# Kernel tuning notes

Measured on AMD Instinct MI355X. Metric: run time of the kernel, lower is better.

The kernel has to match this reference:

```python
import jax, jax.numpy as jnp
import numpy as np

VOCAB = 16000
DIM = 1024
B, T = 4, 2048


def setup_inputs() -> dict:
    key = jax.random.key(0)
    k_ids, k_emb, k_w, k_lw, k_lb = jax.random.split(key, 5)
    input_ids = jax.random.randint(k_ids, (B, T), 0, VOCAB)
    embed = jax.random.normal(k_emb, (VOCAB, DIM), dtype=jnp.float32)
    # w_state = I + 0.05 * (default Linear init ~ U(-1/sqrt(dim), 1/sqrt(dim)))
    bound = 1.0 / np.sqrt(DIM)
    w_state = jnp.eye(DIM, dtype=jnp.float32) + 0.05 * jax.random.uniform(
        k_w, (DIM, DIM), minval=-bound, maxval=bound, dtype=jnp.float32)
    lm_w = jax.random.uniform(k_lw, (VOCAB, DIM), minval=-bound, maxval=bound, dtype=jnp.float32)
    lm_b = jax.random.uniform(k_lb, (VOCAB,), minval=-bound, maxval=bound, dtype=jnp.float32)
    return {"input_ids": input_ids, "embed": embed, "w_state": w_state,
            "lm_w": lm_w, "lm_b": lm_b}


def reference(input_ids, embed, w_state, lm_w, lm_b):
    # h: [B, T, D]
    h = embed[input_ids]
    state0 = jnp.zeros((h.shape[0], h.shape[2]), dtype=h.dtype)

    def step(state, h_t):
        # nn.Linear: state @ W^T ; then add input injection
        new_state = state @ w_state.T + h_t
        return new_state, new_state

    # scan over time: inputs [T, B, D]
    _, outs = jax.lax.scan(step, state0, jnp.swapaxes(h, 0, 1))
    hidden = jnp.swapaxes(outs, 0, 1)  # [B, T, D]
    logits = hidden @ lm_w.T + lm_b    # [B, T, V]
    return logits
```

## Files before the change

kernel.cpp:

```cpp
#include <hip/hip_runtime.h>
#include <hip/hip_bf16.h>
#include <stdint.h>

#define DD 1024
#define BB 4
#define TT 2048
#define VV 16000
#define LCH 8
#define NR 1024
#define PADR 512
#define NPAD 16128

typedef __bf16 bf16_t;
typedef float f32x4_t __attribute__((ext_vector_type(4)));
typedef bf16_t bf16x8_t __attribute__((ext_vector_type(8)));
typedef bf16_t bf16x4_t __attribute__((ext_vector_type(4)));

#define MODE_PLAIN 0
#define MODE_ROUND 1
#define MODE_LEVEL 2
#define MODE_CARRY 3

#define KIND_SQ 0
#define KIND_ROUND 1
#define KIND_LEVEL 2
#define KIND_CARRY 3

struct Job {
  const float* A; const float* B; float* C; const float* Cin;
  int kind; int dlt;
};
struct Jobs { Job j[8]; };

__global__ __launch_bounds__(256) void k_cvt(const float* __restrict__ src,
                                             bf16_t* __restrict__ dst, int n4) {
  int i = blockIdx.x * blockDim.x + threadIdx.x;
  int stride = gridDim.x * blockDim.x;
  for (; i < n4; i += stride) {
    float4 v = ((const float4*)src)[i];
    union { ushort4 u; bf16_t h[4]; } p;
    p.h[0] = (bf16_t)v.x; p.h[1] = (bf16_t)v.y;
    p.h[2] = (bf16_t)v.z; p.h[3] = (bf16_t)v.w;
    ((ushort4*)dst)[i] = p.u;
  }
}

__global__ __launch_bounds__(256) void k_gather(const float* __restrict__ embed,
                                                const int* __restrict__ ids,
                                                float* __restrict__ slab0) {
  int r = blockIdx.x;
  int b = r & 3, c = r >> 2;
  int id = ids[b * TT + c * LCH];
  const float4* s = (const float4*)(embed + (size_t)id * DD);
  float4* d = (float4*)(slab0 + (size_t)r * DD);
  for (int i = threadIdx.x; i < DD / 4; i += blockDim.x) d[i] = s[i];
}

template <int NS>
__device__ __forceinline__ void swrite(char* base, int byteoff, float4 v) {
  float r0 = v.x, r1 = v.y, r2 = v.z, r3 = v.w;
#pragma unroll
  for (int p = 0; p < NS; ++p) {
    bf16x4_t h;
    h[0] = (bf16_t)r0; h[1] = (bf16_t)r1; h[2] = (bf16_t)r2; h[3] = (bf16_t)r3;
    *(bf16x4_t*)(base + p * 5120 + byteoff) = h;
    if (p + 1 < NS) {
      r0 -= (float)h[0]; r1 -= (float)h[1]; r2 -= (float)h[2]; r3 -= (float)h[3];
    }
  }
}

template <int NS, bool NN, int MODE>
__device__ __forceinline__ void mbody(bf16_t* __restrict__ SB, const Job& jb,
                                      const float* __restrict__ embed,
                                      const int* __restrict__ ids,
                                      bf16_t* __restrict__ hidden) {
  const float* A = jb.A;
  const float* Bm = jb.B;
  const int tid = threadIdx.x, lane = tid & 63, wave = tid >> 6;
  const int i0 = blockIdx.y * 64, j0 = blockIdx.x * 64;
  const int wm = (wave >> 1) * 32, wn = (wave & 1) * 32;
  char* Ap = (char*)SB;
  char* Bp = Ap + NS * 5120;
  const int arow = tid >> 2;
  const int akb = (tid & 3) * 8;
  const int bj = tid & 63, bk4 = (tid >> 6) * 4;
  const int frow = lane & 15, fkb = (lane >> 4) * 16;
  f32x4_t acc[2][2] = {};

  const float* Aptr = A + (size_t)(i0 + arow) * DD + (tid & 3) * 4;
  const float* BptrNT = Bm + (size_t)(j0 + arow) * DD + (tid & 3) * 4;
  const float* BptrNN = Bm + (size_t)bk4 * DD + j0 + bj;

  float4 a0 = *(const float4*)(Aptr);
  float4 a1 = *(const float4*)(Aptr + 16);
  float4 b0, b1;
  float s0[4], s1[4];
  if (!NN) {
    b0 = *(const float4*)(BptrNT);
    b1 = *(const float4*)(BptrNT + 16);
  } else {
#pragma unroll
    for (int s = 0; s < 4; ++s) s0[s] = BptrNN[(size_t)s * DD];
#pragma unroll
    for (int s = 0; s < 4; ++s) s1[s] = BptrNN[(size_t)(16 + s) * DD];
  }

  for (int k0 = 0;;) {
    __syncthreads();
    swrite<NS>(Ap, arow * 80 + akb, a0);
    swrite<NS>(Ap, arow * 80 + akb + 32, a1);
    if (!NN) {
      swrite<NS>(Bp, arow * 80 + akb, b0);
      swrite<NS>(Bp, arow * 80 + akb + 32, b1);
    } else {
      float4 t0; t0.x = s0[0]; t0.y = s0[1]; t0.z = s0[2]; t0.w = s0[3];
      float4 t1; t1.x = s1[0]; t1.y = s1[1]; t1.z = s1[2]; t1.w = s1[3];
      swrite<NS>(Bp, bj * 80 + bk4 * 2, t0);
      swrite<NS>(Bp, bj * 80 + bk4 * 2 + 32, t1);
    }
    __syncthreads();
    int kn = k0 + 32;
    if (kn < DD) {
      a0 = *(const float4*)(Aptr + kn);
      a1 = *(const float4*)(Aptr + kn + 16);
      if (!NN) {
        b0 = *(const float4*)(BptrNT + kn);
        b1 = *(const float4*)(BptrNT + kn + 16);
      } else {
#pragma unroll
        for (int s = 0; s < 4; ++s) s0[s] = BptrNN[(size_t)(kn + s) * DD];
#pragma unroll
        for (int s = 0; s < 4; ++s) s1[s] = BptrNN[(size_t)(kn + 16 + s) * DD];
      }
    }
    bf16x8_t af[NS][2], bfx[NS][2];
#pragma unroll
    for (int p = 0; p < NS; ++p)
#pragma unroll
      for (int mf = 0; mf < 2; ++mf) {
        af[p][mf] = *(const bf16x8_t*)(Ap + p * 5120 + (wm + mf * 16 + frow) * 80 + fkb);
        bfx[p][mf] = *(const bf16x8_t*)(Bp + p * 5120 + (wn + mf * 16 + frow) * 80 + fkb);
      }
#pragma unroll
    for (int pa = 0; pa < NS; ++pa)
#pragma unroll
      for (int pb = 0; pb < NS; ++pb) {
        if (pa + pb < NS) {
#pragma unroll
          for (int mf = 0; mf < 2; ++mf)
#pragma unroll
            for (int nf = 0; nf < 2; ++nf)
              acc[mf][nf] = __builtin_amdgcn_mfma_f32_16x16x32_bf16(
                  af[pa][mf], bfx[pb][nf], acc[mf][nf], 0, 0, 0);
        }
      }
    k0 = kn;
    if (k0 >= DD) break;
  }

  const int ecol = lane & 15, er4 = (lane >> 4) * 4;
#pragma unroll
  for (int mf = 0; mf < 2; ++mf) {
#pragma unroll
    for (int nf = 0; nf < 2; ++nf) {
      const int rb = i0 + wm + mf * 16 + er4;
      const int cj = j0 + wn + nf * 16 + ecol;
#pragma unroll
      for (int rg = 0; rg < 4; ++rg) {
        const int ri = rb + rg;
        float v = acc[mf][nf][rg];
        if (MODE == MODE_PLAIN) {
          jb.C[(size_t)ri * DD + cj] = v;
        } else if (MODE == MODE_ROUND) {
          int b = ri & 3, c = ri >> 2, t = c * LCH + jb.dlt;
          v += embed[(size_t)ids[b * TT + t] * DD + cj];
          jb.C[(size_t)ri * DD + cj] = v;
        } else if (MODE == MODE_LEVEL) {
          v += jb.Cin[(size_t)ri * DD + cj];
          jb.C[(size_t)ri * DD + cj] = v;
        } else {
          int b = ri & 3, c = ri >> 2, t = c * LCH + jb.dlt;
          hidden[((size_t)b * TT + t) * DD + cj] =
              (bf16_t)(v + jb.Cin[(size_t)ri * DD + cj]);
        }
      }
    }
  }
}

__global__ __launch_bounds__(256, 2) void k_multi(Jobs jobs,
                                                  const float* __restrict__ embed,
                                                  const int* __restrict__ ids,
                                                  bf16_t* __restrict__ hidden) {
  __shared__ __align__(16) bf16_t SB[6 * 2560];
  const Job& jb = jobs.j[blockIdx.z];
  if (jb.kind == KIND_SQ)
    mbody<3, true, MODE_PLAIN>(SB, jb, embed, ids, hidden);
  else if (jb.kind == KIND_ROUND)
    mbody<2, false, MODE_ROUND>(SB, jb, embed, ids, hidden);
  else if (jb.kind == KIND_LEVEL)
    mbody<2, false, MODE_LEVEL>(SB, jb, embed, ids, hidden);
  else
    mbody<2, false, MODE_CARRY>(SB, jb, embed, ids, hidden);
}

__device__ __forceinline__ void gload16(const void* g, void* l) {
  __builtin_amdgcn_global_load_lds((const __attribute__((address_space(1))) void*)g,
                                   (__attribute__((address_space(3))) void*)l, 16, 0, 0);
}

#define NTK 32

__global__ __launch_bounds__(512, 2) void k_lmhead2(
    const bf16_t* __restrict__ Ah, const bf16_t* __restrict__ Bw,
    const float* __restrict__ bias, float* __restrict__ Cout) {
  __shared__ __align__(16) char LB[4 * 32768];
  const int tid = threadIdx.x, lane = tid & 63, wave = tid >> 6;
  const int wr = wave >> 2, wc = wave & 3;
  int orig = blockIdx.y * gridDim.x + blockIdx.x;
  int swz = (orig & 7) * 252 + (orig >> 3);
  int by = swz / 63, bx = swz % 63;
  const int m0 = by * 256, n0 = bx * 256;

  const int srow = tid >> 2;
  const int scb = (tid & 3) * 16;

  auto stage = [&](int t) {
    char* buf = LB + (size_t)(t & 3) * 32768;
#pragma unroll
    for (int p = 0; p < 2; ++p) {
      int row = p * 128 + srow;
      int sw = ((row >> 1) & 3) << 4;
      gload16((const char*)Ah + ((size_t)(m0 + row) * DD + t * 32) * 2 + (scb ^ sw),
              buf + p * 8192 + wave * 1024);
      gload16((const char*)Bw + ((size_t)(n0 + row) * DD + t * 32) * 2 + (scb ^ sw),
              buf + 16384 + p * 8192 + wave * 1024);
    }
  };

  const int frow = lane & 15;
  const int c4b = (lane >> 4) * 16;
  f32x4_t acc[8][4] = {};

  stage(0); stage(1); stage(2);
  asm volatile("s_waitcnt vmcnt(8)\ns_barrier" ::: "memory");

  for (int t = 0; t < NTK; ++t) {
    char* Abuf = LB + (size_t)(t & 3) * 32768;
    char* Bbuf = Abuf + 16384;
    if (t + 3 < NTK) stage(t + 3);
    bf16x8_t afr[4], bfr[4];
#pragma unroll
    for (int nf = 0; nf < 4; ++nf) {
      int r = wc * 64 + nf * 16 + frow;
      bfr[nf] = *(const bf16x8_t*)(Bbuf + r * 64 + (c4b ^ (((r >> 1) & 3) << 4)));
    }
#pragma unroll
    for (int mf = 0; mf < 4; ++mf) {
      int r = wr * 128 + mf * 16 + frow;
      afr[mf] = *(const bf16x8_t*)(Abuf + r * 64 + (c4b ^ (((r >> 1) & 3) << 4)));
    }
    __builtin_amdgcn_s_setprio(1);
#pragma unroll
    for (int mf = 0; mf < 4; ++mf)
#pragma unroll
      for (int nf = 0; nf < 4; ++nf)
        acc[mf][nf] = __builtin_amdgcn_mfma_f32_16x16x32_bf16(
            afr[mf], bfr[nf], acc[mf][nf], 0, 0, 0);
    __builtin_amdgcn_s_setprio(0);
#pragma unroll
    for (int mf = 0; mf < 4; ++mf) {
      int r = wr * 128 + 64 + mf * 16 + frow;
      afr[mf] = *(const bf16x8_t*)(Abuf + r * 64 + (c4b ^ (((r >> 1) & 3) << 4)));
    }
    __builtin_amdgcn_s_setprio(1);
#pragma unroll
    for (int mf = 0; mf < 4; ++mf)
#pragma unroll
      for (int nf = 0; nf < 4; ++nf)
        acc[4 + mf][nf] = __builtin_amdgcn_mfma_f32_16x16x32_bf16(
            afr[mf], bfr[nf], acc[4 + mf][nf], 0, 0, 0);
    __builtin_amdgcn_s_setprio(0);
    if (t < NTK - 3) {
      asm volatile("s_waitcnt vmcnt(8)\ns_barrier" ::: "memory");
    } else if (t == NTK - 3) {
      asm volatile("s_waitcnt vmcnt(4)\ns_barrier" ::: "memory");
    } else if (t == NTK - 2) {
      asm volatile("s_waitcnt vmcnt(0)\ns_barrier" ::: "memory");
    }
  }

  const int ecol = lane & 15, er4 = (lane >> 4) * 4;
#pragma unroll
  for (int mf = 0; mf < 8; ++mf) {
#pragma unroll
    for (int nf = 0; nf < 4; ++nf) {
      int gm = m0 + wr * 128 + mf * 16 + er4;
      int gn = n0 + wc * 64 + nf * 16 + ecol;
      if (gn < VV) {
        float bv = bias[gn];
#pragma unroll
        for (int rg = 0; rg < 4; ++rg)
          Cout[(size_t)(gm + rg) * VV + gn] = acc[mf][nf][rg] + bv;
      }
    }
  }
}

extern "C" void kernel_launch(void* const* d_in, const int* in_sizes, int n_in,
                              void* d_out, int out_size, void* d_ws, size_t ws_size,
                              hipStream_t stream) {
  (void)in_sizes; (void)n_in; (void)out_size; (void)ws_size;
  const int* ids = (const int*)d_in[0];
  const float* embed = (const float*)d_in[1];
  const float* w_state = (const float*)d_in[2];
  const float* lm_w = (const float*)d_in[3];
  const float* lm_b = (const float*)d_in[4];
  float* out = (float*)d_out;

  const size_t M1 = (size_t)DD * DD;
  float* PW = (float*)d_ws;
  float* Q = PW + 8 * M1;
  float* LOC = Q + 7 * M1;
  float* E0 = LOC + 8 * M1;
  float* E1 = E0 + (size_t)(PADR + NR) * DD;
  bf16_t* HID = (bf16_t*)(E1 + (size_t)(PADR + NR) * DD);
  bf16_t* LWB = HID + (size_t)BB * TT * DD;
  float* E0d = E0 + (size_t)PADR * DD;
  float* E1d = E1 + (size_t)PADR * DD;

  k_cvt<<<2048, 256, 0, stream>>>(lm_w, LWB, VV * DD / 4);
  hipMemsetAsync(LWB + (size_t)VV * DD, 0,
                 (size_t)(NPAD - VV) * DD * sizeof(bf16_t), stream);
  hipMemcpyAsync(PW, w_state, M1 * sizeof(float), hipMemcpyDeviceToDevice, stream);
  k_gather<<<NR, 256, 0, stream>>>(embed, ids, LOC);
  hipMemsetAsync(E0, 0, (size_t)PADR * DD * sizeof(float), stream);
  hipMemsetAsync(E1, 0, (size_t)PADR * DD * sizeof(float), stream);

  Jobs J{};
  J.j[0] = Job{w_state, w_state, PW + M1, nullptr, KIND_SQ, 0};
  J.j[1] = Job{LOC, w_state, LOC + M1, nullptr, KIND_ROUND, 1};
  k_multi<<<dim3(16, 16, 2), 256, 0, stream>>>(J, embed, ids, HID);
  J.j[0] = Job{PW + M1, w_state, PW + 2 * M1, nullptr, KIND_SQ, 0};
  J.j[1] = Job{PW + M1, PW + M1, PW + 3 * M1, nullptr, KIND_SQ, 0};
  J.j[2] = Job{LOC + M1, w_state, LOC + 2 * M1, nullptr, KIND_ROUND, 2};
  k_multi<<<dim3(16, 16, 3), 256, 0, stream>>>(J, embed, ids, HID);
  J.j[0] = Job{PW + 3 * M1, w_state, PW + 4 * M1, nullptr, KIND_SQ, 0};
  J.j[1] = Job{PW + 3 * M1, PW + M1, PW + 5 * M1, nullptr, KIND_SQ, 0};
  J.j[2] = Job{PW + 3 * M1, PW + 2 * M1, PW + 6 * M1, nullptr, KIND_SQ, 0};
  J.j[3] = Job{PW + 3 * M1, PW + 3 * M1, PW + 7 * M1, nullptr, KIND_SQ, 0};
  J.j[4] = Job{LOC + 2 * M1, w_state, LOC + 3 * M1, nullptr, KIND_ROUND, 3};
  k_multi<<<dim3(16, 16, 5), 256, 0, stream>>>(J, embed, ids, HID);
  for (int d = 4; d <= 7; ++d) {
    const float* src = (d == 4) ? (PW + 7 * M1) : (Q + (size_t)(d - 5) * M1);
    J.j[0] = Job{src, src, Q + (size_t)(d - 4) * M1, nullptr, KIND_SQ, 0};
    J.j[1] = Job{LOC + (size_t)(d - 1) * M1, w_state, LOC + (size_t)d * M1,
                 nullptr, KIND_ROUND, d};
    k_multi<<<dim3(16, 16, 2), 256, 0, stream>>>(J, embed, ids, HID);
  }
  hipMemcpyAsync(E0d, LOC + 7 * M1, M1 * sizeof(float),
                 hipMemcpyDeviceToDevice, stream);

  float* inp = E0d;
  float* outp = E1d;
  for (int k = 0; k < 8; ++k) {
    Jobs J2{};
    int nz = 0;
    if (k <= 2) {
      const float* src = Q + (size_t)(k + 3) * M1;
      J2.j[nz++] = Job{src, src, Q + (size_t)(k + 4) * M1, nullptr, KIND_SQ, 0};
    }
    const float* Bq = (k == 0) ? (PW + 7 * M1) : (Q + (size_t)(k - 1) * M1);
    J2.j[nz++] = Job{inp - (size_t)(4 << k) * DD, Bq, outp, inp, KIND_LEVEL, 0};
    k_multi<<<dim3(16, 16, nz), 256, 0, stream>>>(J2, embed, ids, HID);
    float* t = inp; inp = outp; outp = t;
  }

  Jobs Jc{};
  for (int d = 0; d < 8; ++d)
    Jc.j[d] = Job{inp - (size_t)4 * DD, PW + (size_t)d * M1, nullptr,
                  LOC + (size_t)d * M1, KIND_CARRY, d};
  k_multi<<<dim3(16, 16, 8), 256, 0, stream>>>(Jc, embed, ids, HID);

  dim3 gl(NPAD / 256, (BB * TT) / 256);
  k_lmhead2<<<gl, 512, 0, stream>>>(HID, LWB, lm_b, out);
}
```

Baseline: 900.1 us.

## Store recurrence powers and states as pre-split bf16 pieces with async LDS loads

Adds a new path that keeps the power matrices, chunk states and level buffers as pre-split bf16 hi/mid/lo pieces, written in both row- and column-major form, instead of fp32 that was split on every tile load. The GEMM tiles are loaded with global_load_lds into swizzled LDS, and the triple-bf16 product is done with 6 MFMA terms for the power squaring and 3 terms for the state jobs. This cuts global traffic and per-tile conversion work and raises occupancy to 3 blocks per CU. In exchange it needs a much larger workspace, falls back to the old path when the workspace is too small, and stores states with only two bf16 pieces, which may lose some accuracy.

```diff
diff --git a/kernel.cpp b/kernel.cpp
--- a/kernel.cpp
+++ b/kernel.cpp
@@ -10,27 +10,28 @@
 #define NR 1024
 #define PADR 512
 #define NPAD 16128
+#define M1C ((size_t)DD * DD)
+#define ESTR ((PADR + NR) * DD)
 
 typedef __bf16 bf16_t;
 typedef float f32x4_t __attribute__((ext_vector_type(4)));
 typedef bf16_t bf16x8_t __attribute__((ext_vector_type(8)));
 typedef bf16_t bf16x4_t __attribute__((ext_vector_type(4)));
 
-#define MODE_PLAIN 0
-#define MODE_ROUND 1
-#define MODE_LEVEL 2
-#define MODE_CARRY 3
-
 #define KIND_SQ 0
 #define KIND_ROUND 1
 #define KIND_LEVEL 2
 #define KIND_CARRY 3
 
-struct Job {
-  const float* A; const float* B; float* C; const float* Cin;
-  int kind; int dlt;
-};
-struct Jobs { Job j[8]; };
+__device__ __forceinline__ void gload16(const void* g, void* l) {
+  __builtin_amdgcn_global_load_lds((const __attribute__((address_space(1))) void*)g,
+                                   (__attribute__((address_space(3))) void*)l, 16, 0, 0);
+}
+
+__device__ __forceinline__ void split3(float v, bf16_t& h0, bf16_t& h1, bf16_t& h2) {
+  h0 = (bf16_t)v; float r = v - (float)h0;
+  h1 = (bf16_t)r; h2 = (bf16_t)(r - (float)h1);
+}
 
 __global__ __launch_bounds__(256) void k_cvt(const float* __restrict__ src,
                                              bf16_t* __restrict__ dst, int n4) {
@@ -45,9 +46,240 @@
   }
 }
 
-__global__ __launch_bounds__(256) void k_gather(const float* __restrict__ embed,
-                                                const int* __restrict__ ids,
-                                                float* __restrict__ slab0) {
+struct Job {
+  const void* A; const void* B; void* C; void* C2; const void* Cin;
+  int kind, dlt, astr, cinstr, cstr;
+};
+struct Jobs { Job j[8]; };
+
+__global__ __launch_bounds__(256) void k_prepW(const float* __restrict__ W,
+                                               bf16_t* __restrict__ Wrow,
+                                               bf16_t* __restrict__ Wcol) {
+  __shared__ float t[32][33];
+  int bx = blockIdx.x * 32, by = blockIdx.y * 32;
+  int tx = threadIdx.x & 31, ty = threadIdx.x >> 5;
+#pragma unroll
+  for (int q = 0; q < 4; ++q) {
+    int r = by + ty + q * 8;
+    float v = W[(size_t)r * DD + bx + tx];
+    t[ty + q * 8][tx] = v;
+    bf16_t h0, h1, h2; split3(v, h0, h1, h2);
+    size_t o = (size_t)r * DD + bx + tx;
+    Wrow[o] = h0; Wrow[o + M1C] = h1; Wrow[o + 2 * M1C] = h2;
+  }
+  __syncthreads();
+#pragma unroll
+  for (int q = 0; q < 4; ++q) {
+    float v = t[tx][ty + q * 8];
+    bf16_t h0, h1, h2; split3(v, h0, h1, h2);
+    size_t o = (size_t)(bx + ty + q * 8) * DD + by + tx;
+    Wcol[o] = h0; Wcol[o + M1C] = h1; Wcol[o + 2 * M1C] = h2;
+  }
+}
+
+__global__ __launch_bounds__(256) void k_gather2(const float* __restrict__ embed,
+                                                 const int* __restrict__ ids,
+                                                 bf16_t* __restrict__ slab0) {
+  int r = blockIdx.x;
+  int b = r & 3, c = r >> 2;
+  int id = ids[b * TT + c * LCH];
+  const float4* s = (const float4*)(embed + (size_t)id * DD);
+  bf16_t* p0 = slab0 + (size_t)r * DD;
+  bf16_t* p1 = p0 + M1C;
+  for (int i = threadIdx.x; i < DD / 4; i += blockDim.x) {
+    float4 v = s[i];
+    union { ushort4 u; bf16_t h[4]; } a, bq;
+    a.h[0] = (bf16_t)v.x; bq.h[0] = (bf16_t)(v.x - (float)a.h[0]);
+    a.h[1] = (bf16_t)v.y; bq.h[1] = (bf16_t)(v.y - (float)a.h[1]);
+    a.h[2] = (bf16_t)v.z; bq.h[2] = (bf16_t)(v.z - (float)a.h[2]);
+    a.h[3] = (bf16_t)v.w; bq.h[3] = (bf16_t)(v.w - (float)a.h[3]);
+    ((ushort4*)p0)[i] = a.u;
+    ((ushort4*)p1)[i] = bq.u;
+  }
+}
+
+template <bool SQ6>
+__device__ __forceinline__ void tbody(char* SB, const Job& jb,
+                                      const float* __restrict__ embed,
+                                      const int* __restrict__ ids) {
+  constexpr int BK = SQ6 ? 32 : 64;
+  constexpr int NP = SQ6 ? 3 : 2;
+  constexpr int ROWB = BK * 2;
+  constexpr int PTB = 64 * ROWB;
+  const bf16_t* Ab = (const bf16_t*)jb.A;
+  const bf16_t* Bb = (const bf16_t*)jb.B;
+  const int tid = threadIdx.x, lane = tid & 63, wave = tid >> 6;
+  const int i0 = blockIdx.y * 64, j0 = blockIdx.x * 64;
+  const int wm = (wave >> 1) * 32, wn = (wave & 1) * 32;
+  char* BL = SB + NP * PTB;
+  const int frow = lane & 15, fq = lane >> 4;
+  f32x4_t acc[2][2] = {};
+
+  for (int kt = 0; kt < DD / BK; ++kt) {
+    const int k0 = kt * BK;
+    __syncthreads();
+    if (SQ6) {
+      const int row = tid >> 2, g = tid & 3;
+      const int gs = g ^ ((row >> 1) & 3);
+#pragma unroll
+      for (int p = 0; p < 3; ++p) {
+        gload16(Ab + (size_t)p * jb.astr + (size_t)(i0 + row) * DD + k0 + gs * 8,
+                SB + p * PTB + wave * 1024);
+        gload16(Bb + (size_t)p * M1C + (size_t)(j0 + row) * DD + k0 + gs * 8,
+                BL + p * PTB + wave * 1024);
+      }
+    } else {
+      const int row8 = tid >> 3, g = tid & 7;
+#pragma unroll
+      for (int p = 0; p < 2; ++p)
+#pragma unroll
+        for (int h = 0; h < 2; ++h) {
+          int row = h * 32 + row8;
+          int gs = g ^ (row & 7);
+          gload16(Ab + (size_t)p * jb.astr + (size_t)(i0 + row) * DD + k0 + gs * 8,
+                  SB + p * PTB + h * 4096 + wave * 1024);
+          gload16(Bb + (size_t)p * M1C + (size_t)(j0 + row) * DD + k0 + gs * 8,
+                  BL + p * PTB + h * 4096 + wave * 1024);
+        }
+    }
+    asm volatile("s_waitcnt vmcnt(0)" ::: "memory");
+    __syncthreads();
+
+    if (SQ6) {
+      bf16x8_t af[3][2], bfx[3][2];
+#pragma unroll
+      for (int p = 0; p < 3; ++p)
+#pragma unroll
+        for (int mf = 0; mf < 2; ++mf) {
+          int ra = wm + mf * 16 + frow;
+          af[p][mf] = *(const bf16x8_t*)(SB + p * PTB + ra * 64 +
+                                         ((fq ^ ((ra >> 1) & 3)) << 4));
+          int rb = wn + mf * 16 + frow;
+          bfx[p][mf] = *(const bf16x8_t*)(BL + p * PTB + rb * 64 +
+                                          ((fq ^ ((rb >> 1) & 3)) << 4));
+        }
+      const int TA[6] = {0, 0, 1, 0, 2, 1}, TB[6] = {0, 1, 0, 2, 0, 1};
+#pragma unroll
+      for (int tix = 0; tix < 6; ++tix)
+#pragma unroll
+        for (int mf = 0; mf < 2; ++mf)
+#pragma unroll
+          for (int nf = 0; nf < 2; ++nf)
+            acc[mf][nf] = __builtin_amdgcn_mfma_f32_16x16x32_bf16(
+                af[TA[tix]][mf], bfx[TB[tix]][nf], acc[mf][nf], 0, 0, 0);
+    } else {
+      bf16x8_t af[2][2][2], bfx[2][2][2];
+#pragma unroll
+      for (int p = 0; p < 2; ++p)
+#pragma unroll
+        for (int mf = 0; mf < 2; ++mf)
+#pragma unroll
+          for (int ks = 0; ks < 2; ++ks) {
+            int ra = wm + mf * 16 + frow;
+            af[p][mf][ks] = *(const bf16x8_t*)(SB + p * PTB + ra * 128 +
+                                               (((ks * 4 + fq) ^ (ra & 7)) << 4));
+            int rb = wn + mf * 16 + frow;
+            bfx[p][mf][ks] = *(const bf16x8_t*)(BL + p * PTB + rb * 128 +
+                                                (((ks * 4 + fq) ^ (rb & 7)) << 4));
+          }
+#pragma unroll
+      for (int ks = 0; ks < 2; ++ks)
+#pragma unroll
+        for (int mf = 0; mf < 2; ++mf)
+#pragma unroll
+          for (int nf = 0; nf < 2; ++nf) {
+            acc[mf][nf] = __builtin_amdgcn_mfma_f32_16x16x32_bf16(
+                af[0][mf][ks], bfx[0][nf][ks], acc[mf][nf], 0, 0, 0);
+            acc[mf][nf] = __builtin_amdgcn_mfma_f32_16x16x32_bf16(
+                af[0][mf][ks], bfx[1][nf][ks], acc[mf][nf], 0, 0, 0);
+            acc[mf][nf] = __builtin_amdgcn_mfma_f32_16x16x32_bf16(
+                af[1][mf][ks], bfx[0][nf][ks], acc[mf][nf], 0, 0, 0);
+          }
+    }
+  }
+
+  const int ecol = lane & 15, er4 = fq * 4;
+#pragma unroll
+  for (int mf = 0; mf < 2; ++mf) {
+#pragma unroll
+    for (int nf = 0; nf < 2; ++nf) {
+      const int rb0 = i0 + wm + mf * 16 + er4;
+      const int cj = j0 + wn + nf * 16 + ecol;
+      if (SQ6) {
+        bf16_t* Cr = (bf16_t*)jb.C;
+        bf16x4_t c0, c1, c2;
+#pragma unroll
+        for (int rg = 0; rg < 4; ++rg) {
+          float v = acc[mf][nf][rg];
+          bf16_t h0, h1, h2; split3(v, h0, h1, h2);
+          size_t o = (size_t)(rb0 + rg) * DD + cj;
+          Cr[o] = h0; Cr[o + M1C] = h1; Cr[o + 2 * M1C] = h2;
+          c0[rg] = h0; c1[rg] = h1; c2[rg] = h2;
+        }
+        if (jb.C2) {
+          bf16_t* Cc = (bf16_t*)jb.C2;
+          size_t o = (size_t)cj * DD + rb0;
+          *(bf16x4_t*)(Cc + o) = c0;
+          *(bf16x4_t*)(Cc + o + M1C) = c1;
+          *(bf16x4_t*)(Cc + o + 2 * M1C) = c2;
+        }
+      } else if (jb.kind == KIND_ROUND) {
+        bf16_t* Cr = (bf16_t*)jb.C;
+#pragma unroll
+        for (int rg = 0; rg < 4; ++rg) {
+          int ri = rb0 + rg;
+          int b = ri & 3, c = ri >> 2, t = c * LCH + jb.dlt;
+          float v = acc[mf][nf][rg] + embed[(size_t)ids[b * TT + t] * DD + cj];
+          bf16_t h0 = (bf16_t)v;
+          size_t o = (size_t)ri * DD + cj;
+          Cr[o] = h0; Cr[o + jb.cstr] = (bf16_t)(v - (float)h0);
+        }
+      } else if (jb.kind == KIND_LEVEL) {
+        bf16_t* Cr = (bf16_t*)jb.C;
+        const bf16_t* Ci = (const bf16_t*)jb.Cin;
+#pragma unroll
+        for (int rg = 0; rg < 4; ++rg) {
+          int ri = rb0 + rg;
+          size_t o = (size_t)ri * DD + cj;
+          float cin = (float)Ci[o] + (float)Ci[o + jb.cinstr];
+          float v = acc[mf][nf][rg] + cin;
+          bf16_t h0 = (bf16_t)v;
+          Cr[o] = h0; Cr[o + jb.cstr] = (bf16_t)(v - (float)h0);
+        }
+      } else {
+        bf16_t* Hid = (bf16_t*)jb.C;
+        const bf16_t* Ci = (const bf16_t*)jb.Cin;
+#pragma unroll
+        for (int rg = 0; rg < 4; ++rg) {
+          int ri = rb0 + rg;
+          int b = ri & 3, c = ri >> 2, t = c * LCH + jb.dlt;
+          size_t o = (size_t)ri * DD + cj;
+          float cin = (float)Ci[o] + (float)Ci[o + jb.cinstr];
+          Hid[((size_t)b * TT + t) * DD + cj] = (bf16_t)(acc[mf][nf][rg] + cin);
+        }
+      }
+    }
+  }
+}
+
+__global__ __launch_bounds__(256, 3) void k_multi2(Jobs jobs,
+                                                   const float* __restrict__ embed,
+                                                   const int* __restrict__ ids) {
+  __shared__ __align__(16) char SB[32768];
+  const Job& jb = jobs.j[blockIdx.z];
+  if (jb.kind == KIND_SQ) tbody<true>(SB, jb, embed, ids);
+  else tbody<false>(SB, jb, embed, ids);
+}
+
+struct JobF {
+  const float* A; const float* B; float* C; const float* Cin;
+  int kind; int dlt;
+};
+struct JobsF { JobF j[8]; };
+
+__global__ __launch_bounds__(256) void k_gatherF(const float* __restrict__ embed,
+                                                 const int* __restrict__ ids,
+                                                 float* __restrict__ slab0) {
   int r = blockIdx.x;
   int b = r & 3, c = r >> 2;
   int id = ids[b * TT + c * LCH];
@@ -71,16 +303,16 @@
 }
 
 template <int NS, bool NN, int MODE>
-__device__ __forceinline__ void mbody(bf16_t* __restrict__ SB, const Job& jb,
-                                      const float* __restrict__ embed,
-                                      const int* __restrict__ ids,
-                                      bf16_t* __restrict__ hidden) {
+__device__ __forceinline__ void mbodyF(bf16_t* __restrict__ SBb, const JobF& jb,
+                                       const float* __restrict__ embed,
+                                       const int* __restrict__ ids,
+                                       bf16_t* __restrict__ hidden) {
   const float* A = jb.A;
   const float* Bm = jb.B;
   const int tid = threadIdx.x, lane = tid & 63, wave = tid >> 6;
   const int i0 = blockIdx.y * 64, j0 = blockIdx.x * 64;
   const int wm = (wave >> 1) * 32, wn = (wave & 1) * 32;
-  char* Ap = (char*)SB;
+  char* Ap = (char*)SBb;
   char* Bp = Ap + NS * 5120;
   const int arow = tid >> 2;
   const int akb = (tid & 3) * 8;
@@ -170,13 +402,13 @@
       for (int rg = 0; rg < 4; ++rg) {
         const int ri = rb + rg;
         float v = acc[mf][nf][rg];
-        if (MODE == MODE_PLAIN) {
+        if (MODE == 0) {
           jb.C[(size_t)ri * DD + cj] = v;
-        } else if (MODE == MODE_ROUND) {
+        } else if (MODE == 1) {
           int b = ri & 3, c = ri >> 2, t = c * LCH + jb.dlt;
           v += embed[(size_t)ids[b * TT + t] * DD + cj];
           jb.C[(size_t)ri * DD + cj] = v;
-        } else if (MODE == MODE_LEVEL) {
+        } else if (MODE == 2) {
           v += jb.Cin[(size_t)ri * DD + cj];
           jb.C[(size_t)ri * DD + cj] = v;
         } else {
@@ -189,25 +421,20 @@
   }
 }
 
-__global__ __launch_bounds__(256, 2) void k_multi(Jobs jobs,
-                                                  const float* __restrict__ embed,
-                                                  const int* __restrict__ ids,
-                                                  bf16_t* __restrict__ hidden) {
-  __shared__ __align__(16) bf16_t SB[6 * 2560];
-  const Job& jb = jobs.j[blockIdx.z];
+__global__ __launch_bounds__(256, 2) void k_multiF(JobsF jobs,
+                                                   const float* __restrict__ embed,
+                                                   const int* __restrict__ ids,
+                                                   bf16_t* __restrict__ hidden) {
+  __shared__ __align__(16) bf16_t SBb[6 * 2560];
+  const JobF& jb = jobs.j[blockIdx.z];
   if (jb.kind == KIND_SQ)
-    mbody<3, true, MODE_PLAIN>(SB, jb, embed, ids, hidden);
+    mbodyF<3, true, 0>(SBb, jb, embed, ids, hidden);
   else if (jb.kind == KIND_ROUND)
-    mbody<2, false, MODE_ROUND>(SB, jb, embed, ids, hidden);
+    mbodyF<2, false, 1>(SBb, jb, embed, ids, hidden);
   else if (jb.kind == KIND_LEVEL)
-    mbody<2, false, MODE_LEVEL>(SB, jb, embed, ids, hidden);
+    mbodyF<2, false, 2>(SBb, jb, embed, ids, hidden);
   else
-    mbody<2, false, MODE_CARRY>(SB, jb, embed, ids, hidden);
-}
-
-__device__ __forceinline__ void gload16(const void* g, void* l) {
-  __builtin_amdgcn_global_load_lds((const __attribute__((address_space(1))) void*)g,
-                                   (__attribute__((address_space(3))) void*)l, 16, 0, 0);
+    mbodyF<2, false, 3>(SBb, jb, embed, ids, hidden);
 }
 
 #define NTK 32
@@ -308,18 +535,103 @@
   }
 }
 
-extern "C" void kernel_launch(void* const* d_in, const int* in_sizes, int n_in,
-                              void* d_out, int out_size, void* d_ws, size_t ws_size,
-                              hipStream_t stream) {
-  (void)in_sizes; (void)n_in; (void)out_size; (void)ws_size;
-  const int* ids = (const int*)d_in[0];
-  const float* embed = (const float*)d_in[1];
-  const float* w_state = (const float*)d_in[2];
-  const float* lm_w = (const float*)d_in[3];
-  const float* lm_b = (const float*)d_in[4];
-  float* out = (float*)d_out;
-
-  const size_t M1 = (size_t)DD * DD;
+static void run_new(const int* ids, const float* embed, const float* w_state,
+                    const float* lm_w, const float* lm_b, float* out,
+                    void* d_ws, hipStream_t stream) {
+  const size_t M1 = M1C;
+  bf16_t* w = (bf16_t*)d_ws;
+  bf16_t* Wr = w; w += 3 * M1;
+  bf16_t* Wc = w; w += 3 * M1;
+  bf16_t* Pr = w; w += 7 * 3 * M1;
+  bf16_t* Pc2 = w; w += 3 * M1;
+  bf16_t* Pc3 = w; w += 3 * M1;
+  bf16_t* Pc4 = w; w += 3 * M1;
+  bf16_t* Pc8 = w; w += 3 * M1;
+  bf16_t* Qr = w; w += 7 * 3 * M1;
+  bf16_t* Qc = w; w += 6 * 3 * M1;
+  bf16_t* LOCb = w; w += 8 * 2 * M1;
+  bf16_t* E0 = w; w += 2 * (size_t)ESTR;
+  bf16_t* E1 = w; w += 2 * (size_t)ESTR;
+  bf16_t* HID = w; w += (size_t)BB * TT * DD;
+  bf16_t* LWB = w; w += (size_t)NPAD * DD;
+
+  auto PrN = [&](int n) { return Pr + (size_t)(n - 2) * 3 * M1; };
+  auto QrN = [&](int j) { return Qr + (size_t)j * 3 * M1; };
+  auto QcN = [&](int j) { return Qc + (size_t)j * 3 * M1; };
+
+  k_cvt<<<2048, 256, 0, stream>>>(lm_w, LWB, VV * DD / 4);
+  hipMemsetAsync(LWB + (size_t)VV * DD, 0,
+                 (size_t)(NPAD - VV) * DD * sizeof(bf16_t), stream);
+  k_prepW<<<dim3(32, 32), 256, 0, stream>>>(w_state, Wr, Wc);
+  k_gather2<<<NR, 256, 0, stream>>>(embed, ids, LOCb);
+  hipMemsetAsync(E0, 0, 2 * (size_t)ESTR * sizeof(bf16_t), stream);
+  hipMemsetAsync(E1, 0, 2 * (size_t)ESTR * sizeof(bf16_t), stream);
+
+  const int AM1 = (int)M1;
+  auto SQJ = [&](const bf16_t* Arow, const bf16_t* Bcol, bf16_t* Crow, bf16_t* Ccol) {
+    return Job{Arow, Bcol, Crow, Ccol, nullptr, KIND_SQ, 0, AM1, 0, 0};
+  };
+  auto RDJ = [&](int d) {
+    return Job{LOCb + (size_t)(d - 1) * 2 * M1, Wr, LOCb + (size_t)d * 2 * M1,
+               nullptr, nullptr, KIND_ROUND, d, AM1, 0, AM1};
+  };
+
+  Jobs J{};
+  J.j[0] = SQJ(Wr, Wc, PrN(2), Pc2);
+  J.j[1] = RDJ(1);
+  k_multi2<<<dim3(16, 16, 2), 256, 0, stream>>>(J, embed, ids);
+  J.j[0] = SQJ(PrN(2), Wc, PrN(3), Pc3);
+  J.j[1] = SQJ(PrN(2), Pc2, PrN(4), Pc4);
+  J.j[2] = RDJ(2);
+  k_multi2<<<dim3(16, 16, 3), 256, 0, stream>>>(J, embed, ids);
+  J.j[0] = SQJ(PrN(4), Wc, PrN(5), nullptr);
+  J.j[1] = SQJ(PrN(4), Pc2, PrN(6), nullptr);
+  J.j[2] = SQJ(PrN(4), Pc3, PrN(7), nullptr);
+  J.j[3] = SQJ(PrN(4), Pc4, PrN(8), Pc8);
+  J.j[4] = RDJ(3);
+  k_multi2<<<dim3(16, 16, 5), 256, 0, stream>>>(J, embed, ids);
+  for (int d = 4; d <= 7; ++d) {
+    int j = d - 4;
+    if (j == 0) J.j[0] = SQJ(PrN(8), Pc8, QrN(0), QcN(0));
+    else J.j[0] = SQJ(QrN(j - 1), QcN(j - 1), QrN(j), QcN(j));
+    J.j[1] = RDJ(d);
+    k_multi2<<<dim3(16, 16, 2), 256, 0, stream>>>(J, embed, ids);
+  }
+  for (int p = 0; p < 2; ++p)
+    hipMemcpyAsync(E0 + (size_t)p * ESTR + (size_t)PADR * DD,
+                   LOCb + 7 * 2 * M1 + (size_t)p * M1, M1 * sizeof(bf16_t),
+                   hipMemcpyDeviceToDevice, stream);
+
+  bf16_t* inpD = E0 + (size_t)PADR * DD;
+  bf16_t* outD = E1 + (size_t)PADR * DD;
+  for (int k = 0; k < 8; ++k) {
+    Jobs J2{};
+    int nz = 0;
+    if (k <= 2)
+      J2.j[nz++] = SQJ(QrN(k + 3), QcN(k + 3), QrN(k + 4), (k <= 1) ? QcN(k + 4) : nullptr);
+    const bf16_t* Bq = (k == 0) ? PrN(8) : QrN(k - 1);
+    J2.j[nz++] = Job{inpD - (size_t)(4 << k) * DD, Bq, outD, nullptr, inpD,
+                     KIND_LEVEL, 0, (int)ESTR, (int)ESTR, (int)ESTR};
+    k_multi2<<<dim3(16, 16, nz), 256, 0, stream>>>(J2, embed, ids);
+    bf16_t* t = inpD; inpD = outD; outD = t;
+  }
+
+  Jobs Jc{};
+  for (int d = 0; d < 8; ++d) {
+    const bf16_t* Bd = (d == 0) ? Wr : PrN(d + 1);
+    Jc.j[d] = Job{inpD - (size_t)4 * DD, Bd, HID, nullptr,
+                  LOCb + (size_t)d * 2 * M1, KIND_CARRY, d, (int)ESTR, AM1, 0};
+  }
+  k_multi2<<<dim3(16, 16, 8), 256, 0, stream>>>(Jc, embed, ids);
+
+  dim3 gl(NPAD / 256, (BB * TT) / 256);
+  k_lmhead2<<<gl, 512, 0, stream>>>(HID, LWB, lm_b, out);
+}
+
+static void run_old(const int* ids, const float* embed, const float* w_state,
+                    const float* lm_w, const float* lm_b, float* out,
+                    void* d_ws, hipStream_t stream) {
+  const size_t M1 = M1C;
   float* PW = (float*)d_ws;
   float* Q = PW + 8 * M1;
   float* LOC = Q + 7 * M1;
@@ -334,30 +646,30 @@
   hipMemsetAsync(LWB + (size_t)VV * DD, 0,
                  (size_t)(NPAD - VV) * DD * sizeof(bf16_t), stream);
   hipMemcpyAsync(PW, w_state, M1 * sizeof(float), hipMemcpyDeviceToDevice, stream);
-  k_gather<<<NR, 256, 0, stream>>>(embed, ids, LOC);
+  k_gatherF<<<NR, 256, 0, stream>>>(embed, ids, LOC);
   hipMemsetAsync(E0, 0, (size_t)PADR * DD * sizeof(float), stream);
   hipMemsetAsync(E1, 0, (size_t)PADR * DD * sizeof(float), stream);
 
-  Jobs J{};
-  J.j[0] = Job{w_state, w_state, PW + M1, nullptr, KIND_SQ, 0};
-  J.j[1] = Job{LOC, w_state, LOC + M1, nullptr, KIND_ROUND, 1};
-  k_multi<<<dim3(16, 16, 2), 256, 0, stream>>>(J, embed, ids, HID);
-  J.j[0] = Job{PW + M1, w_state, PW + 2 * M1, nullptr, KIND_SQ, 0};
-  J.j[1] = Job{PW + M1, PW + M1, PW + 3 * M1, nullptr, KIND_SQ, 0};
-  J.j[2] = Job{LOC + M1, w_state, LOC + 2 * M1, nullptr, KIND_ROUND, 2};
-  k_multi<<<dim3(16, 16, 3), 256, 0, stream>>>(J, embed, ids, HID);
-  J.j[0] = Job{PW + 3 * M1, w_state, PW + 4 * M1, nullptr, KIND_SQ, 0};
-  J.j[1] = Job{PW + 3 * M1, PW + M1, PW + 5 * M1, nullptr, KIND_SQ, 0};
-  J.j[2] = Job{PW + 3 * M1, PW + 2 * M1, PW + 6 * M1, nullptr, KIND_SQ, 0};
-  J.j[3] = Job{PW + 3 * M1, PW + 3 * M1, PW + 7 * M1, nullptr, KIND_SQ, 0};
-  J.j[4] = Job{LOC + 2 * M1, w_state, LOC + 3 * M1, nullptr, KIND_ROUND, 3};
-  k_multi<<<dim3(16, 16, 5), 256, 0, stream>>>(J, embed, ids, HID);
+  JobsF J{};
+  J.j[0] = JobF{w_state, w_state, PW + M1, nullptr, KIND_SQ, 0};
+  J.j[1] = JobF{LOC, w_state, LOC + M1, nullptr, KIND_ROUND, 1};
+  k_multiF<<<dim3(16, 16, 2), 256, 0, stream>>>(J, embed, ids, HID);
+  J.j[0] = JobF{PW + M1, w_state, PW + 2 * M1, nullptr, KIND_SQ, 0};
+  J.j[1] = JobF{PW + M1, PW + M1, PW + 3 * M1, nullptr, KIND_SQ, 0};
+  J.j[2] = JobF{LOC + M1, w_state, LOC + 2 * M1, nullptr, KIND_ROUND, 2};
+  k_multiF<<<dim3(16, 16, 3), 256, 0, stream>>>(J, embed, ids, HID);
+  J.j[0] = JobF{PW + 3 * M1, w_state, PW + 4 * M1, nullptr, KIND_SQ, 0};
+  J.j[1] = JobF{PW + 3 * M1, PW + M1, PW + 5 * M1, nullptr, KIND_SQ, 0};
+  J.j[2] = JobF{PW + 3 * M1, PW + 2 * M1, PW + 6 * M1, nullptr, KIND_SQ, 0};
+  J.j[3] = JobF{PW + 3 * M1, PW + 3 * M1, PW + 7 * M1, nullptr, KIND_SQ, 0};
+  J.j[4] = JobF{LOC + 2 * M1, w_state, LOC + 3 * M1, nullptr, KIND_ROUND, 3};
+  k_multiF<<<dim3(16, 16, 5), 256, 0, stream>>>(J, embed, ids, HID);
   for (int d = 4; d <= 7; ++d) {
     const float* src = (d == 4) ? (PW + 7 * M1) : (Q + (size_t)(d - 5) * M1);
-    J.j[0] = Job{src, src, Q + (size_t)(d - 4) * M1, nullptr, KIND_SQ, 0};
-    J.j[1] = Job{LOC + (size_t)(d - 1) * M1, w_state, LOC + (size_t)d * M1,
-                 nullptr, KIND_ROUND, d};
-    k_multi<<<dim3(16, 16, 2), 256, 0, stream>>>(J, embed, ids, HID);
+    J.j[0] = JobF{src, src, Q + (size_t)(d - 4) * M1, nullptr, KIND_SQ, 0};
+    J.j[1] = JobF{LOC + (size_t)(d - 1) * M1, w_state, LOC + (size_t)d * M1,
+                  nullptr, KIND_ROUND, d};
+    k_multiF<<<dim3(16, 16, 2), 256, 0, stream>>>(J, embed, ids, HID);
   }
   hipMemcpyAsync(E0d, LOC + 7 * M1, M1 * sizeof(float),
                  hipMemcpyDeviceToDevice, stream);
@@ -365,24 +677,44 @@
   float* inp = E0d;
   float* outp = E1d;
   for (int k = 0; k < 8; ++k) {
-    Jobs J2{};
+    JobsF J2{};
     int nz = 0;
     if (k <= 2) {
       const float* src = Q + (size_t)(k + 3) * M1;
-      J2.j[nz++] = Job{src, src, Q + (size_t)(k + 4) * M1, nullptr, KIND_SQ, 0};
+      J2.j[nz++] = JobF{src, src, Q + (size_t)(k + 4) * M1, nullptr, KIND_SQ, 0};
     }
     const float* Bq = (k == 0) ? (PW + 7 * M1) : (Q + (size_t)(k - 1) * M1);
-    J2.j[nz++] = Job{inp - (size_t)(4 << k) * DD, Bq, outp, inp, KIND_LEVEL, 0};
-    k_multi<<<dim3(16, 16, nz), 256, 0, stream>>>(J2, embed, ids, HID);
+    J2.j[nz++] = JobF{inp - (size_t)(4 << k) * DD, Bq, outp, inp, KIND_LEVEL, 0};
+    k_multiF<<<dim3(16, 16, nz), 256, 0, stream>>>(J2, embed, ids, HID);
     float* t = inp; inp = outp; outp = t;
   }
 
-  Jobs Jc{};
+  JobsF Jc{};
   for (int d = 0; d < 8; ++d)
-    Jc.j[d] = Job{inp - (size_t)4 * DD, PW + (size_t)d * M1, nullptr,
-                  LOC + (size_t)d * M1, KIND_CARRY, d};
-  k_multi<<<dim3(16, 16, 8), 256, 0, stream>>>(Jc, embed, ids, HID);
+    Jc.j[d] = JobF{inp - (size_t)4 * DD, PW + (size_t)d * M1, nullptr,
+                   LOC + (size_t)d * M1, KIND_CARRY, d};
+  k_multiF<<<dim3(16, 16, 8), 256, 0, stream>>>(Jc, embed, ids, HID);
 
   dim3 gl(NPAD / 256, (BB * TT) / 256);
   k_lmhead2<<<gl, 512, 0, stream>>>(HID, LWB, lm_b, out);
 }
+
+extern "C" void kernel_launch(void* const* d_in, const int* in_sizes, int n_in,
+                              void* d_out, int out_size, void* d_ws, size_t ws_size,
+                              hipStream_t stream) {
+  (void)in_sizes; (void)n_in; (void)out_size;
+  const int* ids = (const int*)d_in[0];
+  const float* embed = (const float*)d_in[1];
+  const float* w_state = (const float*)d_in[2];
+  const float* lm_w = (const float*)d_in[3];
+  const float* lm_b = (const float*)d_in[4];
+  float* out = (float*)d_out;
+
+  const size_t needNew =
+      (94 * M1C + 4 * (size_t)ESTR + (size_t)BB * TT * DD + (size_t)NPAD * DD) *
+      sizeof(bf16_t);
+  if (ws_size >= needNew)
+    run_new(ids, embed, w_state, lm_w, lm_b, out, d_ws, stream);
+  else
+    run_old(ids, embed, w_state, lm_w, lm_b, out, d_ws, stream);
+}
```

Result: no change. 888.9 us (-1.2%).
